# Kernel tuning notes

Hardware: AMD Instinct MI355X
Metric: run time of the kernel (lower is better)

Reference implementation:

```python
import jax, jax.numpy as jnp
import numpy as np

HEADS = 8
Q_DIM = 128
V_DIM = 128
OUT_DIM = 128
SCALE = OUT_DIM ** (-0.5)


def _lrelu(x):
    return jnp.where(x >= 0, x, 0.01 * x)


def _gelu(x):
    return jax.nn.gelu(x, approximate=False)


def setup_inputs() -> dict:
    key = jax.random.key(0)
    ks = iter(jax.random.split(key, 32))
    B, H, W, N = 4, 32, 32, 2048
    p = lambda *s: jax.random.normal(next(ks), s, dtype=jnp.float32) * 0.02
    return {
        "query": jax.random.normal(next(ks), (B, Q_DIM, H, W), dtype=jnp.float32),
        "fts": jax.random.normal(next(ks), (B * HEADS, V_DIM, N), dtype=jnp.float32),
        # 1x1 conv proj_q_c: Conv2d(q_dim, q_dim*heads)
        "wqc": p(Q_DIM * HEADS, Q_DIM), "bqc": p(Q_DIM * HEADS),
        # proj_q_l: Linear(q,q) -> LeakyReLU -> Linear(q,out) -> GELU
        "wq1": p(Q_DIM, Q_DIM), "bq1": p(Q_DIM),
        "wq2": p(OUT_DIM, Q_DIM), "bq2": p(OUT_DIM),
        # proj_k
        "wk1": p(V_DIM, V_DIM), "bk1": p(V_DIM),
        "wk2": p(OUT_DIM, V_DIM), "bk2": p(OUT_DIM),
        # proj_v
        "wv1": p(V_DIM, V_DIM), "bv1": p(V_DIM),
        "wv2": p(OUT_DIM, V_DIM), "bv2": p(OUT_DIM),
        # proj_out 1x1 conv (out_dim -> out_dim)
        "wo": p(OUT_DIM, OUT_DIM), "bo": p(OUT_DIM),
        # final_out: Linear(out*heads, out) -> LReLU -> Linear(out,out) -> LReLU
        "wf1": p(OUT_DIM, OUT_DIM * HEADS), "bf1": p(OUT_DIM),
        "wf2": p(OUT_DIM, OUT_DIM), "bf2": p(OUT_DIM),
    }


def reference(query, fts, wqc, bqc, wq1, bq1, wq2, bq2, wk1, bk1, wk2, bk2,
              wv1, bv1, wv2, bv2, wo, bo, wf1, bf1, wf2, bf2):
    B, C, H, W = query.shape
    # 1x1 conv q projection: [B, heads*q_dim, H, W]
    q1 = jnp.einsum('bchw,oc->bohw', query, wqc) + bqc[None, :, None, None]
    # rearrange 'b (h c) l w -> (b h) (l w) c'
    qh = q1.reshape(B, HEADS, C, H, W).transpose(0, 1, 3, 4, 2).reshape(B * HEADS, H * W, C)
    q = _gelu(_lrelu(qh @ wq1.T + bq1) @ wq2.T + bq2)            # [B*h, HW, D]
    ft = fts.transpose(0, 2, 1)                                   # [B*h, N, v_dim]
    k = _gelu(_lrelu(ft @ wk1.T + bk1) @ wk2.T + bk2)             # [B*h, N, D]
    v = _gelu(_lrelu(ft @ wv1.T + bv1) @ wv2.T + bv2)             # [B*h, N, D]
    attn = jax.nn.softmax(jnp.einsum('bmd,bnd->bmn', q, k) * SCALE, axis=-1)
    enh = jnp.einsum('bmn,bnd->bmd', attn, v)                     # [B*h, HW, D]
    enh4 = enh.transpose(0, 2, 1).reshape(B * HEADS, OUT_DIM, H, W)
    ho = jnp.einsum('bdhw,od->bohw', enh4, wo) + bo[None, :, None, None]
    # rearrange '(b h) c l w -> b l w (h c)'
    x = ho.reshape(B, HEADS, OUT_DIM, H, W).transpose(0, 3, 4, 1, 2).reshape(B, H, W, HEADS * OUT_DIM)
    out = _lrelu(_lrelu(x @ wf1.T + bf1) @ wf2.T + bf2)           # [B, H, W, D]
    return out
```

## Files before the change

kernel.cpp:

```cpp
#include <hip/hip_runtime.h>
#include <math.h>

typedef __attribute__((ext_vector_type(8))) __bf16 bf16x8;
typedef __attribute__((ext_vector_type(4))) float f32x4;
typedef __attribute__((ext_vector_type(4))) unsigned u32x4;

__device__ __forceinline__ float act_lrelu(float x) { return x >= 0.0f ? x : 0.01f * x; }
__device__ __forceinline__ float act_gelu(float x) { return 0.5f * x * (1.0f + erff(x * 0.7071067811865475f)); }
__device__ __forceinline__ ushort f2bf(float f) {
    unsigned u = __builtin_bit_cast(unsigned, f);
    u += 0x7fffu + ((u >> 16) & 1u);
    return (ushort)(u >> 16);
}
__device__ __forceinline__ unsigned pack2bf(float lo, float hi) {
    return (unsigned)f2bf(lo) | ((unsigned)f2bf(hi) << 16);
}

__device__ __forceinline__ void stage_wbf(const ushort* __restrict__ Wg,
                                          ushort* Wl, int tid)
{
    #pragma unroll
    for (int it = 0; it < 8; ++it) {
        const int lin = (tid + it * 256) * 8;
        const int r = lin >> 7, c = lin & 127;
        const bf16x8 v = *(const bf16x8*)&Wg[lin];
        *(bf16x8*)&Wl[r * 128 + (c ^ ((r & 7) << 3))] = v;
    }
}

__device__ __forceinline__ void layer8swz(const bf16x8 a[4], const ushort* Wl,
                                          f32x4 acc[8], int l15, int lk8)
{
    const int sx = (l15 & 7) << 3;
    #pragma unroll
    for (int ds = 0; ds < 4; ++ds) {
        const int cb = (ds * 32 + lk8) ^ sx;
        #pragma unroll
        for (int nt = 0; nt < 8; ++nt) {
            const bf16x8 b = *(const bf16x8*)&Wl[(nt * 16 + l15) * 128 + cb];
            acc[nt] = __builtin_amdgcn_mfma_f32_16x16x32_bf16(a[ds], b, acc[nt], 0, 0, 0);
        }
    }
}

template <int ACT>
__device__ __forceinline__ void retile_swz(const f32x4 acc[8], const float bias[8],
                                           ushort* tlw, int l15, int lr4, int lk8,
                                           bf16x8 aout[4])
{
    #pragma unroll
    for (int nt = 0; nt < 8; ++nt)
        #pragma unroll
        for (int j = 0; j < 4; ++j) {
            float v = acc[nt][j] + bias[nt];
            if constexpr (ACT == 1) v = act_lrelu(v);
            if constexpr (ACT == 2) v = act_gelu(v);
            const int row = lr4 + j;
            tlw[row * 128 + ((nt * 16 + l15) ^ ((row & 7) << 3))] = f2bf(v);
        }
    const int sx = (l15 & 7) << 3;
    #pragma unroll
    for (int ds = 0; ds < 4; ++ds)
        aout[ds] = *(const bf16x8*)&tlw[l15 * 128 + ((ds * 32 + lk8) ^ sx)];
}

__device__ __forceinline__ void transpose_tile(
    const float* __restrict__ IN, ushort* __restrict__ OUTb,
    int C, int N, int bx, int by, int bz, float (*T)[68], int tid)
{
    const int r = tid >> 4, c4 = (tid & 15) * 4;
    const int n0 = bx * 64, c0 = by * 64;
    const size_t ib = (size_t)bz * C * N;
    const size_t ob = (size_t)bz * N * C;
    #pragma unroll
    for (int p = 0; p < 4; ++p) {
        const int cl = r + p * 16;
        const float4 v = *(const float4*)&IN[ib + (size_t)(c0 + cl) * N + n0 + c4];
        *(float4*)&T[cl][c4] = v;
    }
    __syncthreads();
    #pragma unroll
    for (int p = 0; p < 4; ++p) {
        const int nl = r + p * 16;
        ushort4 u;
        u.x = f2bf(T[c4 + 0][nl]);
        u.y = f2bf(T[c4 + 1][nl]);
        u.z = f2bf(T[c4 + 2][nl]);
        u.w = f2bf(T[c4 + 3][nl]);
        *(ushort4*)&OUTb[ob + (size_t)(n0 + nl) * C + c0 + c4] = u;
    }
}

__global__ __launch_bounds__(256) void prep_kernel(
    const float* __restrict__ wqc, const float* __restrict__ wq1,
    const float* __restrict__ wq2, const float* __restrict__ wk1,
    const float* __restrict__ wk2, const float* __restrict__ wv1,
    const float* __restrict__ wv2, const float* __restrict__ wf2,
    const float* __restrict__ query, const float* __restrict__ fts,
    const float* __restrict__ wo, const float* __restrict__ wf1,
    const float* __restrict__ bo, const float* __restrict__ bf1,
    ushort* __restrict__ Wdst, ushort* __restrict__ queryT,
    ushort* __restrict__ ftb, ushort* __restrict__ Wcomb,
    float* __restrict__ bconst)
{
    __shared__ __align__(16) char sbuf[32768];
    const int tid = threadIdx.x;
    const int blk = blockIdx.x;

    if (blk < 60) {
        #pragma unroll
        for (int p = 0; p < 4; ++p) {
            const int lin = blk * 4096 + p * 1024 + tid * 4;
            const float* s;
            if (lin < 131072) s = wqc + lin;
            else {
                const int m = (lin - 131072) >> 14, idx = (lin - 131072) & 16383;
                s = (m == 0) ? wq1 + idx : (m == 1) ? wq2 + idx : (m == 2) ? wk1 + idx :
                    (m == 3) ? wk2 + idx : (m == 4) ? wv1 + idx : (m == 5) ? wv2 + idx
                             : wf2 + idx;
            }
            const float4 v = *(const float4*)s;
            ushort4 u; u.x = f2bf(v.x); u.y = f2bf(v.y); u.z = f2bf(v.z); u.w = f2bf(v.w);
            *(ushort4*)&Wdst[lin] = u;
        }
    } else if (blk < 188) {
        const int b2 = blk - 60;
        transpose_tile(query, queryT, 128, 1024, b2 & 15, (b2 >> 4) & 1, b2 >> 5,
                       (float(*)[68])sbuf, tid);
    } else if (blk < 196) {
        ushort* Wl = (ushort*)sbuf;
        const int h = blk - 188;
        const int lane = tid & 63, w = tid >> 6;
        const int l15 = lane & 15, lk8 = (lane >> 4) * 8, lr4 = (lane >> 4) * 4;
        #pragma unroll
        for (int it = 0; it < 16; ++it) {
            const int lin = (tid + it * 256) * 4;
            const int o = lin >> 7, d4 = lin & 127;
            const float4 v = *(const float4*)&wo[o * 128 + d4];
            #pragma unroll
            for (int j = 0; j < 4; ++j) {
                const int d = d4 + j;
                Wl[d * 128 + (o ^ ((d & 7) << 3))] = f2bf((&v.x)[j]);
            }
        }
        __syncthreads();
        const f32x4 z = {0.f, 0.f, 0.f, 0.f};
        #pragma unroll
        for (int rf = 0; rf < 2; ++rf) {
            const int row = w * 32 + rf * 16;
            bf16x8 a[4];
            #pragma unroll
            for (int ds = 0; ds < 4; ++ds) {
                const size_t base = (size_t)(row + l15) * 1024 + h * 128 + ds * 32 + lk8;
                const float4 lo = *(const float4*)&wf1[base];
                const float4 hi = *(const float4*)&wf1[base + 4];
                u32x4 wv;
                wv[0] = pack2bf(lo.x, lo.y); wv[1] = pack2bf(lo.z, lo.w);
                wv[2] = pack2bf(hi.x, hi.y); wv[3] = pack2bf(hi.z, hi.w);
                a[ds] = __builtin_bit_cast(bf16x8, wv);
            }
            f32x4 acc[8];
            #pragma unroll
            for (int i = 0; i < 8; ++i) acc[i] = z;
            layer8swz(a, Wl, acc, l15, lk8);
            #pragma unroll
            for (int nt = 0; nt < 8; ++nt)
                #pragma unroll
                for (int j = 0; j < 4; ++j)
                    Wcomb[h * 16384 + (row + lr4 + j) * 128 + nt * 16 + l15] =
                        f2bf(acc[nt][j]);
        }
    } else if (blk < 200) {
        float* sm = (float*)sbuf;
        const int jl = tid >> 3, part = tid & 7;
        const int j = (blk - 196) * 32 + jl;
        float4 a4 = {0.f, 0.f, 0.f, 0.f};
        #pragma unroll
        for (int kk = 0; kk < 128; kk += 4) {
            const float4 wv = *(const float4*)&wf1[(size_t)j * 1024 + part * 128 + kk];
            const float4 bv = *(const float4*)&bo[kk];
            a4.x += wv.x * bv.x; a4.y += wv.y * bv.y;
            a4.z += wv.z * bv.z; a4.w += wv.w * bv.w;
        }
        sm[tid] = a4.x + a4.y + a4.z + a4.w;
        __syncthreads();
        if (part == 0) {
            float t = bf1[j];
            #pragma unroll
            for (int p2 = 0; p2 < 8; ++p2) t += sm[jl * 8 + p2];
            bconst[j] = t;
        }
    } else {
        const int b2 = blk - 200;
        transpose_tile(fts, ftb, 128, 2048, b2 & 31, (b2 >> 5) & 1, b2 >> 6,
                       (float(*)[68])sbuf, tid);
    }
}

__global__ __launch_bounds__(256) void mlp1v(
    const ushort* __restrict__ X, const ushort* __restrict__ Wbf,
    const float* __restrict__ Bf, ushort* __restrict__ Y)
{
    __shared__ ushort Wl[128 * 128];
    const int tid = threadIdx.x, lane = tid & 63, w = tid >> 6;
    const int l15 = lane & 15, lk8 = (lane >> 4) * 8, lr4 = (lane >> 4) * 4;
    const int head = (blockIdx.x >> 3) & 7;
    stage_wbf(Wbf + head * 16384, Wl, tid);
    float b0[8];
    #pragma unroll
    for (int nt = 0; nt < 8; ++nt) b0[nt] = Bf[head * 128 + nt * 16 + l15];

    const int m0 = blockIdx.x * 128 + w * 32;
    bf16x8 a0[4], a1[4];
    #pragma unroll
    for (int ds = 0; ds < 4; ++ds) {
        int r0 = m0 + l15, r1 = m0 + 16 + l15;
        r0 = (r0 >> 13) * 1024 + (r0 & 1023);
        r1 = (r1 >> 13) * 1024 + (r1 & 1023);
        a0[ds] = *(const bf16x8*)(X + (size_t)r0 * 128 + ds * 32 + lk8);
        a1[ds] = *(const bf16x8*)(X + (size_t)r1 * 128 + ds * 32 + lk8);
    }
    __syncthreads();
    const f32x4 z = {0.f, 0.f, 0.f, 0.f};
    #pragma unroll
    for (int rf = 0; rf < 2; ++rf) {
        f32x4 acc[8];
        #pragma unroll
        for (int i = 0; i < 8; ++i) acc[i] = z;
        layer8swz(rf ? a1 : a0, Wl, acc, l15, lk8);
        const int row = m0 + rf * 16;
        #pragma unroll
        for (int nt = 0; nt < 8; ++nt)
            #pragma unroll
            for (int j = 0; j < 4; ++j)
                Y[(size_t)(row + lr4 + j) * 128 + nt * 16 + l15] = f2bf(acc[nt][j] + b0[nt]);
    }
}

__global__ __launch_bounds__(256) void mlp2dual(
    const ushort* __restrict__ qh, const ushort* __restrict__ ftb,
    const ushort* __restrict__ Wbf,
    const float* __restrict__ bq1, const float* __restrict__ bq2,
    const float* __restrict__ bk1, const float* __restrict__ bk2,
    const float* __restrict__ bv1, const float* __restrict__ bv2,
    ushort* __restrict__ qbuf, ushort* __restrict__ kbuf,
    ushort* __restrict__ vbufT)
{
    __shared__ ushort W1l[128 * 128], W2l[128 * 128];
    __shared__ ushort tl[4][16 * 128];
    const int tid = threadIdx.x, lane = tid & 63, w = tid >> 6;
    const int l15 = lane & 15, lk8 = (lane >> 4) * 8, lr4 = (lane >> 4) * 4;
    const int blk = blockIdx.x;

    const ushort *X, *W1, *W2;
    const float *B1, *B2;
    ushort* Y;
    bool outt = false;
    int m0;
    if (blk < 256) {
        X = qh;  W1 = Wbf + 131072; W2 = Wbf + 147456; B1 = bq1; B2 = bq2;
        Y = qbuf;  m0 = blk * 128;
    } else if (blk < 768) {
        X = ftb; W1 = Wbf + 163840; W2 = Wbf + 180224; B1 = bk1; B2 = bk2;
        Y = kbuf;  m0 = (blk - 256) * 128;
    } else {
        X = ftb; W1 = Wbf + 196608; W2 = Wbf + 212992; B1 = bv1; B2 = bv2;
        Y = vbufT; m0 = (blk - 768) * 128; outt = true;
    }
    stage_wbf(W1, W1l, tid);
    stage_wbf(W2, W2l, tid);
    float b1[8], b2[8];
    #pragma unroll
    for (int nt = 0; nt < 8; ++nt) { b1[nt] = B1[nt * 16 + l15]; b2[nt] = B2[nt * 16 + l15]; }

    const int mw = m0 + w * 32;
    bf16x8 a0[4], a1[4];
    #pragma unroll
    for (int ds = 0; ds < 4; ++ds) {
        a0[ds] = *(const bf16x8*)(X + (size_t)(mw + l15) * 128 + ds * 32 + lk8);
        a1[ds] = *(const bf16x8*)(X + (size_t)(mw + 16 + l15) * 128 + ds * 32 + lk8);
    }
    __syncthreads();
    const f32x4 z = {0.f, 0.f, 0.f, 0.f};
    #pragma unroll
    for (int rf = 0; rf < 2; ++rf) {
        const int row = mw + rf * 16;
        f32x4 acc[8];
        #pragma unroll
        for (int i = 0; i < 8; ++i) acc[i] = z;
        layer8swz(rf ? a1 : a0, W1l, acc, l15, lk8);
        bf16x8 a2[4];
        retile_swz<1>(acc, b1, tl[w], l15, lr4, lk8, a2);
        f32x4 acc2[8];
        #pragma unroll
        for (int i = 0; i < 8; ++i) acc2[i] = z;
        layer8swz(a2, W2l, acc2, l15, lk8);
        if (!outt) {
            #pragma unroll
            for (int nt = 0; nt < 8; ++nt)
                #pragma unroll
                for (int j = 0; j < 4; ++j)
                    Y[(size_t)(row + lr4 + j) * 128 + nt * 16 + l15] =
                        f2bf(act_gelu(acc2[nt][j] + b2[nt]));
        } else {
            const int R0 = row + lr4;
            const int bh = R0 >> 11, key = R0 & 2047;
            #pragma unroll
            for (int nt = 0; nt < 8; ++nt) {
                ushort4 pk;
                #pragma unroll
                for (int j = 0; j < 4; ++j)
                    (&pk.x)[j] = f2bf(act_gelu(acc2[nt][j] + b2[nt]));
                *(ushort4*)&Y[((size_t)bh * 128 + nt * 16 + l15) * 2048 + key] = pk;
            }
        }
    }
}

__global__ __launch_bounds__(128) void outpath2(
    const ushort* __restrict__ E, const ushort* __restrict__ Wcomb,
    const float* __restrict__ bconst, const ushort* __restrict__ Wf2bf,
    const float* __restrict__ Bf2, float* __restrict__ OUT)
{
    __shared__ ushort Wc[128 * 128], W2l[128 * 128];
    __shared__ ushort tl[2][16 * 128];
    const int tid = threadIdx.x, lane = tid & 63, w = tid >> 6;
    const int l15 = lane & 15, lk8 = (lane >> 4) * 8, lr4 = (lane >> 4) * 4;
    const int b = blockIdx.x >> 5;
    const int m0 = (blockIdx.x & 31) * 32;

    #pragma unroll
    for (int it = 0; it < 16; ++it) {
        const int lin = (tid + it * 128) * 8;
        const int r = lin >> 7, c = lin & 127;
        *(bf16x8*)&W2l[r * 128 + (c ^ ((r & 7) << 3))] = *(const bf16x8*)&Wf2bf[lin];
    }
    float bc[8], b2[8];
    #pragma unroll
    for (int nt = 0; nt < 8; ++nt) { bc[nt] = bconst[nt * 16 + l15]; b2[nt] = Bf2[nt * 16 + l15]; }

    const f32x4 z = {0.f, 0.f, 0.f, 0.f};
    f32x4 yacc[8];
    #pragma unroll
    for (int i = 0; i < 8; ++i) yacc[i] = z;

    bf16x8 a[4], an[4], wreg[16];
    auto loadE = [&](int h, bf16x8 dst[4]) {
        const size_t er = ((size_t)((b * 8 + h) * 1024) + m0 + w * 16 + l15) * 128;
        #pragma unroll
        for (int ds = 0; ds < 4; ++ds) dst[ds] = *(const bf16x8*)(E + er + ds * 32 + lk8);
    };
    auto wload = [&](int h) {
        #pragma unroll
        for (int it = 0; it < 16; ++it)
            wreg[it] = *(const bf16x8*)&Wcomb[h * 16384 + (tid + it * 128) * 8];
    };
    auto wwrite = [&]() {
        #pragma unroll
        for (int it = 0; it < 16; ++it) {
            const int lin = (tid + it * 128) * 8;
            const int r = lin >> 7, c = lin & 127;
            *(bf16x8*)&Wc[r * 128 + (c ^ ((r & 7) << 3))] = wreg[it];
        }
    };

    wload(0); wwrite();
    loadE(0, a);
    for (int h = 0; h < 8; ++h) {
        if (h < 7) { wload(h + 1); loadE(h + 1, an); }
        __syncthreads();
        layer8swz(a, Wc, yacc, l15, lk8);
        __syncthreads();
        if (h < 7) {
            wwrite();
            #pragma unroll
            for (int ds = 0; ds < 4; ++ds) a[ds] = an[ds];
        }
    }
    bf16x8 a3[4];
    retile_swz<1>(yacc, bc, tl[w], l15, lr4, lk8, a3);
    f32x4 oacc[8];
    #pragma unroll
    for (int i = 0; i < 8; ++i) oacc[i] = z;
    layer8swz(a3, W2l, oacc, l15, lk8);
    #pragma unroll
    for (int nt = 0; nt < 8; ++nt)
        #pragma unroll
        for (int j = 0; j < 4; ++j)
            OUT[((size_t)b * 1024 + m0 + w * 16 + lr4 + j) * 128 + nt * 16 + l15] =
                act_lrelu(oacc[nt][j] + b2[nt]);
}

__global__ __launch_bounds__(256, 3) void flash_attn_bf16(
    const ushort* __restrict__ Q, const ushort* __restrict__ Kx,
    const ushort* __restrict__ Vt, ushort* __restrict__ O)
{
    constexpr float SCALE = 0.08838834764831845f;
    const int bid = blockIdx.x;
    const int bh = (bid & 7) * 4 + ((bid >> 3) & 3);
    const int m0 = (bid >> 5) * 64;
    const int tid = threadIdx.x;
    const int lane = tid & 63, w = tid >> 6;
    const int l15 = lane & 15, g = lane >> 4;
    const int lk8 = g * 8, lr4 = g * 4;
    const int sxk = (l15 & 7) << 3;
    const int sel = g >> 1;
    const int src0 = l15 + ((lane & 16) << 1);

    __shared__ ushort K_lds[2][64 * 128];
    __shared__ ushort V_lds[128 * 64];

    const ushort* Qb = Q + (size_t)bh * 1024 * 128;
    const ushort* Kb = Kx + (size_t)bh * 2048 * 128;
    const ushort* Vb = Vt + (size_t)bh * 128 * 2048;

    bf16x8 qf[4];
    {
        const int row = m0 + w * 16 + l15;
        #pragma unroll
        for (int ds = 0; ds < 4; ++ds)
            qf[ds] = *(const bf16x8*)(Qb + (size_t)row * 128 + ds * 32 + lk8);
    }

    const int kr = tid >> 4, kc = (tid & 15) * 8;
    const int vr = tid >> 3, vc = (tid & 7) * 8;
    bf16x8 kreg[4], vreg[4];
    #pragma unroll
    for (int it = 0; it < 4; ++it) {
        kreg[it] = *(const bf16x8*)(Kb + (size_t)(kr + it * 16) * 128 + kc);
        vreg[it] = *(const bf16x8*)(Vb + (size_t)(vr + it * 32) * 2048 + vc);
    }
    #pragma unroll
    for (int it = 0; it < 4; ++it) {
        const int r = kr + it * 16;
        *(bf16x8*)&K_lds[0][r * 128 + (kc ^ ((r & 7) << 3))] = kreg[it];
        const int rv = vr + it * 32;
        *(bf16x8*)&V_lds[rv * 64 + (vc ^ ((rv & 7) << 3))] = vreg[it];
    }
    __syncthreads();

    f32x4 oacc[8];
    #pragma unroll
    for (int i = 0; i < 8; ++i) oacc[i] = f32x4{0.f, 0.f, 0.f, 0.f};
    float mrun = -1e30f, lrun = 0.f;
    int cur = 0;

    for (int nt = 0; nt < 32; ++nt) {
        if (nt < 31) {
            const int n1 = (nt + 1) * 64;
            #pragma unroll
            for (int it = 0; it < 4; ++it) {
                kreg[it] = *(const bf16x8*)(Kb + (size_t)(n1 + kr + it * 16) * 128 + kc);
                vreg[it] = *(const bf16x8*)(Vb + (size_t)(vr + it * 32) * 2048 + n1 + vc);
            }
        }
        const ushort* Kc = &K_lds[cur][0];

        f32x4 s[4];
        #pragma unroll
        for (int i = 0; i < 4; ++i) s[i] = f32x4{0.f, 0.f, 0.f, 0.f};
        __builtin_amdgcn_s_setprio(1);
        #pragma unroll
        for (int ds = 0; ds < 4; ++ds)
            #pragma unroll
            for (int ct = 0; ct < 4; ++ct) {
                const bf16x8 kf = *(const bf16x8*)
                    &Kc[(ct * 16 + l15) * 128 + ((ds * 32 + lk8) ^ sxk)];
                s[ct] = __builtin_amdgcn_mfma_f32_16x16x32_bf16(kf, qf[ds], s[ct], 0, 0, 0);
            }
        __builtin_amdgcn_s_setprio(0);

        float mx = fmaxf(fmaxf(fmaxf(s[0][0], s[0][1]), fmaxf(s[0][2], s[0][3])),
                         fmaxf(fmaxf(s[1][0], s[1][1]), fmaxf(s[1][2], s[1][3])));
        mx = fmaxf(mx, fmaxf(fmaxf(fmaxf(s[2][0], s[2][1]), fmaxf(s[2][2], s[2][3])),
                             fmaxf(fmaxf(s[3][0], s[3][1]), fmaxf(s[3][2], s[3][3]))));
        mx *= SCALE;
        mx = fmaxf(mx, __shfl_xor(mx, 16));
        mx = fmaxf(mx, __shfl_xor(mx, 32));

        if (!__all((int)(mx <= mrun + 8.f))) {
            const float mnew = fmaxf(mrun, mx);
            const float fsc = __expf(mrun - mnew);
            mrun = mnew;
            lrun *= fsc;
            #pragma unroll
            for (int dt = 0; dt < 8; ++dt)
                #pragma unroll
                for (int j = 0; j < 4; ++j)
                    oacc[dt][j] *= fsc;
        }

        float p[4][4];
        float sum = 0.f;
        #pragma unroll
        for (int ct = 0; ct < 4; ++ct)
            #pragma unroll
            for (int r = 0; r < 4; ++r) {
                const float e = __expf(s[ct][r] * SCALE - mrun);
                p[ct][r] = e;
                sum += e;
            }
        sum += __shfl_xor(sum, 16);
        sum += __shfl_xor(sum, 32);
        lrun += sum;

        unsigned P2[4][2];
        #pragma unroll
        for (int ct = 0; ct < 4; ++ct) {
            P2[ct][0] = pack2bf(p[ct][0], p[ct][1]);
            P2[ct][1] = pack2bf(p[ct][2], p[ct][3]);
        }

        __builtin_amdgcn_s_setprio(1);
        #pragma unroll
        for (int ks = 0; ks < 2; ++ks) {
            u32x4 wv;
            #pragma unroll
            for (int t = 0; t < 4; ++t) {
                const int src = src0 + ((t >> 1) << 4);
                const unsigned wa = __shfl(P2[ks * 2 + 0][t & 1], src);
                const unsigned wb = __shfl(P2[ks * 2 + 1][t & 1], src);
                wv[t] = sel ? wb : wa;
            }
            const bf16x8 pa = __builtin_bit_cast(bf16x8, wv);
            #pragma unroll
            for (int dt = 0; dt < 8; ++dt) {
                const int rv = dt * 16 + l15;
                const bf16x8 vb = *(const bf16x8*)
                    &V_lds[rv * 64 + ((ks * 32 + lk8) ^ sxk)];
                oacc[dt] = __builtin_amdgcn_mfma_f32_16x16x32_bf16(vb, pa, oacc[dt], 0, 0, 0);
            }
        }
        __builtin_amdgcn_s_setprio(0);

        if (nt < 31) {
            __syncthreads();
            const int nxt = cur ^ 1;
            #pragma unroll
            for (int it = 0; it < 4; ++it) {
                const int r = kr + it * 16;
                *(bf16x8*)&K_lds[nxt][r * 128 + (kc ^ ((r & 7) << 3))] = kreg[it];
                const int rv = vr + it * 32;
                *(bf16x8*)&V_lds[rv * 64 + (vc ^ ((rv & 7) << 3))] = vreg[it];
            }
            __syncthreads();
            cur ^= 1;
        }
    }

    ushort* Ob = O + ((size_t)bh * 1024 + m0 + w * 16 + l15) * 128;
    const float inv = 1.0f / lrun;
    #pragma unroll
    for (int dt = 0; dt < 8; ++dt) {
        ushort4 pk;
        #pragma unroll
        for (int r = 0; r < 4; ++r) (&pk.x)[r] = f2bf(oacc[dt][r] * inv);
        *(ushort4*)&Ob[dt * 16 + lr4] = pk;
    }
}

extern "C" void kernel_launch(void* const* d_in, const int* in_sizes, int n_in,
                              void* d_out, int out_size, void* d_ws, size_t ws_size,
                              hipStream_t stream)
{
    (void)in_sizes; (void)n_in; (void)out_size; (void)ws_size;
    const float* query = (const float*)d_in[0];
    const float* fts   = (const float*)d_in[1];
    const float* wqc = (const float*)d_in[2];
    const float* bqc = (const float*)d_in[3];
    const float* wq1 = (const float*)d_in[4];
    const float* bq1 = (const float*)d_in[5];
    const float* wq2 = (const float*)d_in[6];
    const float* bq2 = (const float*)d_in[7];
    const float* wk1 = (const float*)d_in[8];
    const float* bk1 = (const float*)d_in[9];
    const float* wk2 = (const float*)d_in[10];
    const float* bk2 = (const float*)d_in[11];
    const float* wv1 = (const float*)d_in[12];
    const float* bv1 = (const float*)d_in[13];
    const float* wv2 = (const float*)d_in[14];
    const float* bv2 = (const float*)d_in[15];
    const float* wo  = (const float*)d_in[16];
    const float* bo  = (const float*)d_in[17];
    const float* wf1 = (const float*)d_in[18];
    const float* bf1 = (const float*)d_in[19];
    const float* wf2 = (const float*)d_in[20];
    const float* bf2 = (const float*)d_in[21];
    float* out = (float*)d_out;

    char* ws = (char*)d_ws;
    ushort* ftb    = (ushort*)(ws + 0LL);
    ushort* queryT = (ushort*)(ws + 16777216LL);
    ushort* qh     = (ushort*)(ws + 17825792LL);
    ushort* qbuf   = (ushort*)(ws + 26214400LL);
    ushort* kbuf   = (ushort*)(ws + 34603008LL);
    ushort* vbufT  = (ushort*)(ws + 51380224LL);
    ushort* enh    = (ushort*)(ws + 68157440LL);
    ushort* Wbf    = (ushort*)(ws + 76546048LL);
    ushort* Wcomb  = (ushort*)(ws + 77299712LL);
    float*  bconst = (float*) (ws + 77561856LL);

    ushort* wqc_b = Wbf + 0;
    ushort* wf2_b = Wbf + 229376;

    prep_kernel<<<2248, 256, 0, stream>>>(
        wqc, wq1, wq2, wk1, wk2, wv1, wv2, wf2, query, fts, wo, wf1, bo, bf1,
        Wbf, queryT, ftb, Wcomb, bconst);
    mlp1v<<<256, 256, 0, stream>>>(queryT, wqc_b, bqc, qh);
    mlp2dual<<<1280, 256, 0, stream>>>(qh, ftb, Wbf, bq1, bq2, bk1, bk2,
                                       bv1, bv2, qbuf, kbuf, vbufT);
    flash_attn_bf16<<<512, 256, 0, stream>>>(qbuf, kbuf, vbufT, enh);
    outpath2<<<128, 128, 0, stream>>>(enh, Wcomb, bconst, wf2_b, bf2, out);
}
```

Measured before the change: 182.6 us.

## Fuse q conv projection into the q MLP and split k/v MLPs into separate launches

The 1x1 conv q projection is fused with both q MLP layers into one kernel, so the qh intermediate no longer goes to global memory. The k and v MLPs become a templated kernel launched twice. Blocks grow to 512 threads covering 256 rows, and the second row-fragment's input is prefetched while the first is computed. This removes one kernel's round trip through global memory and some weight restaging, but uses more LDS per block (up to about 128KB for the q kernel), which may lower occupancy, and adds an extra launch for the k/v split.

```diff
diff --git a/kernel.cpp b/kernel.cpp
--- a/kernel.cpp
+++ b/kernel.cpp
@@ -22,6 +22,18 @@
     #pragma unroll
     for (int it = 0; it < 8; ++it) {
         const int lin = (tid + it * 256) * 8;
+        const int r = lin >> 7, c = lin & 127;
+        const bf16x8 v = *(const bf16x8*)&Wg[lin];
+        *(bf16x8*)&Wl[r * 128 + (c ^ ((r & 7) << 3))] = v;
+    }
+}
+
+__device__ __forceinline__ void stage_wbf512(const ushort* __restrict__ Wg,
+                                             ushort* Wl, int tid)
+{
+    #pragma unroll
+    for (int it = 0; it < 4; ++it) {
+        const int lin = (tid + it * 512) * 8;
         const int r = lin >> 7, c = lin & 127;
         const bf16x8 v = *(const bf16x8*)&Wg[lin];
         *(bf16x8*)&Wl[r * 128 + (c ^ ((r & 7) << 3))] = v;
@@ -197,105 +209,114 @@
     }
 }
 
-__global__ __launch_bounds__(256) void mlp1v(
-    const ushort* __restrict__ X, const ushort* __restrict__ Wbf,
-    const float* __restrict__ Bf, ushort* __restrict__ Y)
-{
-    __shared__ ushort Wl[128 * 128];
+__global__ __launch_bounds__(512) void mlp3q(
+    const ushort* __restrict__ Xq, const ushort* __restrict__ Wbf,
+    const float* __restrict__ Bqc, const float* __restrict__ B1,
+    const float* __restrict__ B2, ushort* __restrict__ Y)
+{
+    __shared__ ushort W0l[128 * 128], W1l[128 * 128], W2l[128 * 128];
+    __shared__ ushort tl[8][16 * 128];
     const int tid = threadIdx.x, lane = tid & 63, w = tid >> 6;
     const int l15 = lane & 15, lk8 = (lane >> 4) * 8, lr4 = (lane >> 4) * 4;
-    const int head = (blockIdx.x >> 3) & 7;
-    stage_wbf(Wbf + head * 16384, Wl, tid);
-    float b0[8];
-    #pragma unroll
-    for (int nt = 0; nt < 8; ++nt) b0[nt] = Bf[head * 128 + nt * 16 + l15];
-
-    const int m0 = blockIdx.x * 128 + w * 32;
-    bf16x8 a0[4], a1[4];
-    #pragma unroll
-    for (int ds = 0; ds < 4; ++ds) {
-        int r0 = m0 + l15, r1 = m0 + 16 + l15;
-        r0 = (r0 >> 13) * 1024 + (r0 & 1023);
-        r1 = (r1 >> 13) * 1024 + (r1 & 1023);
-        a0[ds] = *(const bf16x8*)(X + (size_t)r0 * 128 + ds * 32 + lk8);
-        a1[ds] = *(const bf16x8*)(X + (size_t)r1 * 128 + ds * 32 + lk8);
+    const int head = (blockIdx.x >> 2) & 7;
+    stage_wbf512(Wbf + head * 16384, W0l, tid);
+    stage_wbf512(Wbf + 131072, W1l, tid);
+    stage_wbf512(Wbf + 147456, W2l, tid);
+    float b0[8], b1[8], b2[8];
+    #pragma unroll
+    for (int nt = 0; nt < 8; ++nt) {
+        b0[nt] = Bqc[head * 128 + nt * 16 + l15];
+        b1[nt] = B1[nt * 16 + l15];
+        b2[nt] = B2[nt * 16 + l15];
+    }
+
+    const int m0 = blockIdx.x * 256 + w * 32;
+    bf16x8 a[4], an[4];
+    {
+        const int r = (m0 >> 13) * 1024 + (m0 & 1023) + l15;
+        #pragma unroll
+        for (int ds = 0; ds < 4; ++ds)
+            a[ds] = *(const bf16x8*)(Xq + (size_t)r * 128 + ds * 32 + lk8);
     }
     __syncthreads();
     const f32x4 z = {0.f, 0.f, 0.f, 0.f};
     #pragma unroll
     for (int rf = 0; rf < 2; ++rf) {
+        const int row = m0 + rf * 16;
+        if (rf < 1) {
+            const int r = ((row + 16) >> 13) * 1024 + ((row + 16) & 1023) + l15;
+            #pragma unroll
+            for (int ds = 0; ds < 4; ++ds)
+                an[ds] = *(const bf16x8*)(Xq + (size_t)r * 128 + ds * 32 + lk8);
+        }
         f32x4 acc[8];
         #pragma unroll
         for (int i = 0; i < 8; ++i) acc[i] = z;
-        layer8swz(rf ? a1 : a0, Wl, acc, l15, lk8);
-        const int row = m0 + rf * 16;
+        layer8swz(a, W0l, acc, l15, lk8);
+        bf16x8 a1[4];
+        retile_swz<0>(acc, b0, tl[w], l15, lr4, lk8, a1);
+        #pragma unroll
+        for (int i = 0; i < 8; ++i) acc[i] = z;
+        layer8swz(a1, W1l, acc, l15, lk8);
+        bf16x8 a2[4];
+        retile_swz<1>(acc, b1, tl[w], l15, lr4, lk8, a2);
+        #pragma unroll
+        for (int i = 0; i < 8; ++i) acc[i] = z;
+        layer8swz(a2, W2l, acc, l15, lk8);
         #pragma unroll
         for (int nt = 0; nt < 8; ++nt)
             #pragma unroll
             for (int j = 0; j < 4; ++j)
-                Y[(size_t)(row + lr4 + j) * 128 + nt * 16 + l15] = f2bf(acc[nt][j] + b0[nt]);
-    }
-}
-
-__global__ __launch_bounds__(256) void mlp2dual(
-    const ushort* __restrict__ qh, const ushort* __restrict__ ftb,
-    const ushort* __restrict__ Wbf,
-    const float* __restrict__ bq1, const float* __restrict__ bq2,
-    const float* __restrict__ bk1, const float* __restrict__ bk2,
-    const float* __restrict__ bv1, const float* __restrict__ bv2,
-    ushort* __restrict__ qbuf, ushort* __restrict__ kbuf,
-    ushort* __restrict__ vbufT)
+                Y[(size_t)(row + lr4 + j) * 128 + nt * 16 + l15] =
+                    f2bf(act_gelu(acc[nt][j] + b2[nt]));
+        #pragma unroll
+        for (int ds = 0; ds < 4; ++ds) a[ds] = an[ds];
+    }
+}
+
+template <bool OUTT>
+__global__ __launch_bounds__(512) void mlp2v(
+    const ushort* __restrict__ X,
+    const ushort* __restrict__ W1bf, const float* __restrict__ B1,
+    const ushort* __restrict__ W2bf, const float* __restrict__ B2,
+    ushort* __restrict__ Y)
 {
     __shared__ ushort W1l[128 * 128], W2l[128 * 128];
-    __shared__ ushort tl[4][16 * 128];
+    __shared__ ushort tl[8][16 * 128];
     const int tid = threadIdx.x, lane = tid & 63, w = tid >> 6;
     const int l15 = lane & 15, lk8 = (lane >> 4) * 8, lr4 = (lane >> 4) * 4;
-    const int blk = blockIdx.x;
-
-    const ushort *X, *W1, *W2;
-    const float *B1, *B2;
-    ushort* Y;
-    bool outt = false;
-    int m0;
-    if (blk < 256) {
-        X = qh;  W1 = Wbf + 131072; W2 = Wbf + 147456; B1 = bq1; B2 = bq2;
-        Y = qbuf;  m0 = blk * 128;
-    } else if (blk < 768) {
-        X = ftb; W1 = Wbf + 163840; W2 = Wbf + 180224; B1 = bk1; B2 = bk2;
-        Y = kbuf;  m0 = (blk - 256) * 128;
-    } else {
-        X = ftb; W1 = Wbf + 196608; W2 = Wbf + 212992; B1 = bv1; B2 = bv2;
-        Y = vbufT; m0 = (blk - 768) * 128; outt = true;
-    }
-    stage_wbf(W1, W1l, tid);
-    stage_wbf(W2, W2l, tid);
+    stage_wbf512(W1bf, W1l, tid);
+    stage_wbf512(W2bf, W2l, tid);
     float b1[8], b2[8];
     #pragma unroll
     for (int nt = 0; nt < 8; ++nt) { b1[nt] = B1[nt * 16 + l15]; b2[nt] = B2[nt * 16 + l15]; }
 
-    const int mw = m0 + w * 32;
-    bf16x8 a0[4], a1[4];
-    #pragma unroll
-    for (int ds = 0; ds < 4; ++ds) {
-        a0[ds] = *(const bf16x8*)(X + (size_t)(mw + l15) * 128 + ds * 32 + lk8);
-        a1[ds] = *(const bf16x8*)(X + (size_t)(mw + 16 + l15) * 128 + ds * 32 + lk8);
-    }
+    const int m0 = blockIdx.x * 256 + w * 32;
+    bf16x8 a[4], an[4];
+    #pragma unroll
+    for (int ds = 0; ds < 4; ++ds)
+        a[ds] = *(const bf16x8*)(X + (size_t)(m0 + l15) * 128 + ds * 32 + lk8);
     __syncthreads();
     const f32x4 z = {0.f, 0.f, 0.f, 0.f};
     #pragma unroll
     for (int rf = 0; rf < 2; ++rf) {
-        const int row = mw + rf * 16;
+        const int row = m0 + rf * 16;
+        if (rf < 1) {
+            #pragma unroll
+            for (int ds = 0; ds < 4; ++ds)
+                an[ds] = *(const bf16x8*)(X + (size_t)(row + 16 + l15) * 128 + ds * 32 + lk8);
+        }
         f32x4 acc[8];
         #pragma unroll
         for (int i = 0; i < 8; ++i) acc[i] = z;
-        layer8swz(rf ? a1 : a0, W1l, acc, l15, lk8);
+        layer8swz(a, W1l, acc, l15, lk8);
         bf16x8 a2[4];
         retile_swz<1>(acc, b1, tl[w], l15, lr4, lk8, a2);
         f32x4 acc2[8];
         #pragma unroll
         for (int i = 0; i < 8; ++i) acc2[i] = z;
         layer8swz(a2, W2l, acc2, l15, lk8);
-        if (!outt) {
+        if constexpr (!OUTT) {
             #pragma unroll
             for (int nt = 0; nt < 8; ++nt)
                 #pragma unroll
@@ -314,6 +335,8 @@
                 *(ushort4*)&Y[((size_t)bh * 128 + nt * 16 + l15) * 2048 + key] = pk;
             }
         }
+        #pragma unroll
+        for (int ds = 0; ds < 4; ++ds) a[ds] = an[ds];
     }
 }
 
@@ -591,7 +614,6 @@
     char* ws = (char*)d_ws;
     ushort* ftb    = (ushort*)(ws + 0LL);
     ushort* queryT = (ushort*)(ws + 16777216LL);
-    ushort* qh     = (ushort*)(ws + 17825792LL);
     ushort* qbuf   = (ushort*)(ws + 26214400LL);
     ushort* kbuf   = (ushort*)(ws + 34603008LL);
     ushort* vbufT  = (ushort*)(ws + 51380224LL);
@@ -600,15 +622,14 @@
     ushort* Wcomb  = (ushort*)(ws + 77299712LL);
     float*  bconst = (float*) (ws + 77561856LL);
 
-    ushort* wqc_b = Wbf + 0;
     ushort* wf2_b = Wbf + 229376;
 
     prep_kernel<<<2248, 256, 0, stream>>>(
         wqc, wq1, wq2, wk1, wk2, wv1, wv2, wf2, query, fts, wo, wf1, bo, bf1,
         Wbf, queryT, ftb, Wcomb, bconst);
-    mlp1v<<<256, 256, 0, stream>>>(queryT, wqc_b, bqc, qh);
-    mlp2dual<<<1280, 256, 0, stream>>>(qh, ftb, Wbf, bq1, bq2, bk1, bk2,
-                                       bv1, bv2, qbuf, kbuf, vbufT);
+    mlp3q<<<128, 512, 0, stream>>>(queryT, Wbf, bqc, bq1, bq2, qbuf);
+    mlp2v<false><<<256, 512, 0, stream>>>(ftb, Wbf + 163840, bk1, Wbf + 180224, bk2, kbuf);
+    mlp2v<true><<<256, 512, 0, stream>>>(ftb, Wbf + 196608, bv1, Wbf + 212992, bv2, vbufT);
     flash_attn_bf16<<<512, 256, 0, stream>>>(qbuf, kbuf, vbufT, enh);
     outpath2<<<128, 128, 0, stream>>>(enh, Wcomb, bconst, wf2_b, bf2, out);
 }
```

New measurement: 311.0 us. 1.7x slower.

## Split attention over key halves with combine kernel; split fused MLP launch into three

Applied to the files above, without the earlier changes.

The flash attention kernel now splits the 2048 keys into two halves, launching 1024 blocks instead of 512. Each block writes unnormalized fp32 partial outputs plus running max/sum, and a new combine kernel merges them with log-sum-exp weights into the bf16 output. The aim is more parallelism and better CU fill on the attention stage. The cost is roughly 32 MB of extra fp32 partial traffic and one more launch. The merged q/k/v MLP kernel is also replaced by three launches of a templated kernel, which removes the per-block branch but serializes the launches.

```diff
diff --git a/kernel.cpp b/kernel.cpp
--- a/kernel.cpp
+++ b/kernel.cpp
@@ -237,54 +237,35 @@
     }
 }
 
-__global__ __launch_bounds__(256) void mlp2dual(
-    const ushort* __restrict__ qh, const ushort* __restrict__ ftb,
-    const ushort* __restrict__ Wbf,
-    const float* __restrict__ bq1, const float* __restrict__ bq2,
-    const float* __restrict__ bk1, const float* __restrict__ bk2,
-    const float* __restrict__ bv1, const float* __restrict__ bv2,
-    ushort* __restrict__ qbuf, ushort* __restrict__ kbuf,
-    ushort* __restrict__ vbufT)
+template <bool OUTT>
+__global__ __launch_bounds__(256) void mlp2v(
+    const ushort* __restrict__ X,
+    const ushort* __restrict__ W1bf, const float* __restrict__ B1,
+    const ushort* __restrict__ W2bf, const float* __restrict__ B2,
+    ushort* __restrict__ Y)
 {
     __shared__ ushort W1l[128 * 128], W2l[128 * 128];
     __shared__ ushort tl[4][16 * 128];
     const int tid = threadIdx.x, lane = tid & 63, w = tid >> 6;
     const int l15 = lane & 15, lk8 = (lane >> 4) * 8, lr4 = (lane >> 4) * 4;
-    const int blk = blockIdx.x;
-
-    const ushort *X, *W1, *W2;
-    const float *B1, *B2;
-    ushort* Y;
-    bool outt = false;
-    int m0;
-    if (blk < 256) {
-        X = qh;  W1 = Wbf + 131072; W2 = Wbf + 147456; B1 = bq1; B2 = bq2;
-        Y = qbuf;  m0 = blk * 128;
-    } else if (blk < 768) {
-        X = ftb; W1 = Wbf + 163840; W2 = Wbf + 180224; B1 = bk1; B2 = bk2;
-        Y = kbuf;  m0 = (blk - 256) * 128;
-    } else {
-        X = ftb; W1 = Wbf + 196608; W2 = Wbf + 212992; B1 = bv1; B2 = bv2;
-        Y = vbufT; m0 = (blk - 768) * 128; outt = true;
-    }
-    stage_wbf(W1, W1l, tid);
-    stage_wbf(W2, W2l, tid);
+    stage_wbf(W1bf, W1l, tid);
+    stage_wbf(W2bf, W2l, tid);
     float b1[8], b2[8];
     #pragma unroll
     for (int nt = 0; nt < 8; ++nt) { b1[nt] = B1[nt * 16 + l15]; b2[nt] = B2[nt * 16 + l15]; }
 
-    const int mw = m0 + w * 32;
+    const int m0 = blockIdx.x * 128 + w * 32;
     bf16x8 a0[4], a1[4];
     #pragma unroll
     for (int ds = 0; ds < 4; ++ds) {
-        a0[ds] = *(const bf16x8*)(X + (size_t)(mw + l15) * 128 + ds * 32 + lk8);
-        a1[ds] = *(const bf16x8*)(X + (size_t)(mw + 16 + l15) * 128 + ds * 32 + lk8);
+        a0[ds] = *(const bf16x8*)(X + (size_t)(m0 + l15) * 128 + ds * 32 + lk8);
+        a1[ds] = *(const bf16x8*)(X + (size_t)(m0 + 16 + l15) * 128 + ds * 32 + lk8);
     }
     __syncthreads();
     const f32x4 z = {0.f, 0.f, 0.f, 0.f};
     #pragma unroll
     for (int rf = 0; rf < 2; ++rf) {
-        const int row = mw + rf * 16;
+        const int row = m0 + rf * 16;
         f32x4 acc[8];
         #pragma unroll
         for (int i = 0; i < 8; ++i) acc[i] = z;
@@ -295,7 +276,7 @@
         #pragma unroll
         for (int i = 0; i < 8; ++i) acc2[i] = z;
         layer8swz(a2, W2l, acc2, l15, lk8);
-        if (!outt) {
+        if constexpr (!OUTT) {
             #pragma unroll
             for (int nt = 0; nt < 8; ++nt)
                 #pragma unroll
@@ -391,14 +372,17 @@
                 act_lrelu(oacc[nt][j] + b2[nt]);
 }
 
-__global__ __launch_bounds__(256, 3) void flash_attn_bf16(
+__global__ __launch_bounds__(256, 3) void flash_part(
     const ushort* __restrict__ Q, const ushort* __restrict__ Kx,
-    const ushort* __restrict__ Vt, ushort* __restrict__ O)
+    const ushort* __restrict__ Vt, float* __restrict__ Op,
+    float2* __restrict__ ml)
 {
     constexpr float SCALE = 0.08838834764831845f;
     const int bid = blockIdx.x;
     const int bh = (bid & 7) * 4 + ((bid >> 3) & 3);
-    const int m0 = (bid >> 5) * 64;
+    const int ks_half = (bid >> 5) & 1;
+    const int m0 = (bid >> 6) * 64;
+    const int n00 = ks_half * 1024;
     const int tid = threadIdx.x;
     const int lane = tid & 63, w = tid >> 6;
     const int l15 = lane & 15, g = lane >> 4;
@@ -427,8 +411,8 @@
     bf16x8 kreg[4], vreg[4];
     #pragma unroll
     for (int it = 0; it < 4; ++it) {
-        kreg[it] = *(const bf16x8*)(Kb + (size_t)(kr + it * 16) * 128 + kc);
-        vreg[it] = *(const bf16x8*)(Vb + (size_t)(vr + it * 32) * 2048 + vc);
+        kreg[it] = *(const bf16x8*)(Kb + (size_t)(n00 + kr + it * 16) * 128 + kc);
+        vreg[it] = *(const bf16x8*)(Vb + (size_t)(vr + it * 32) * 2048 + n00 + vc);
     }
     #pragma unroll
     for (int it = 0; it < 4; ++it) {
@@ -445,9 +429,9 @@
     float mrun = -1e30f, lrun = 0.f;
     int cur = 0;
 
-    for (int nt = 0; nt < 32; ++nt) {
-        if (nt < 31) {
-            const int n1 = (nt + 1) * 64;
+    for (int nt = 0; nt < 16; ++nt) {
+        if (nt < 15) {
+            const int n1 = n00 + (nt + 1) * 64;
             #pragma unroll
             for (int it = 0; it < 4; ++it) {
                 kreg[it] = *(const bf16x8*)(Kb + (size_t)(n1 + kr + it * 16) * 128 + kc);
@@ -533,7 +517,7 @@
         }
         __builtin_amdgcn_s_setprio(0);
 
-        if (nt < 31) {
+        if (nt < 15) {
             __syncthreads();
             const int nxt = cur ^ 1;
             #pragma unroll
@@ -548,15 +532,43 @@
         }
     }
 
-    ushort* Ob = O + ((size_t)bh * 1024 + m0 + w * 16 + l15) * 128;
-    const float inv = 1.0f / lrun;
-    #pragma unroll
-    for (int dt = 0; dt < 8; ++dt) {
-        ushort4 pk;
-        #pragma unroll
-        for (int r = 0; r < 4; ++r) (&pk.x)[r] = f2bf(oacc[dt][r] * inv);
-        *(ushort4*)&Ob[dt * 16 + lr4] = pk;
-    }
+    const int row = m0 + w * 16 + l15;
+    float* Ob = Op + (size_t)ks_half * 4194304 + ((size_t)bh * 1024 + row) * 128;
+    #pragma unroll
+    for (int dt = 0; dt < 8; ++dt)
+        *(f32x4*)&Ob[dt * 16 + lr4] = oacc[dt];
+    if (g == 0)
+        ml[(size_t)ks_half * 32768 + bh * 1024 + row] = float2{mrun, lrun};
+}
+
+__global__ __launch_bounds__(256) void combine_kernel(
+    const float* __restrict__ Op, const float2* __restrict__ ml,
+    ushort* __restrict__ enh)
+{
+    const int t = threadIdx.x;
+    const int row = blockIdx.x * 16 + (t >> 4);
+    const int d = (t & 15) * 8;
+    const float2 a = ml[row];
+    const float2 b = ml[32768 + row];
+    const float m = fmaxf(a.x, b.x);
+    const float w1 = __expf(a.x - m), w2 = __expf(b.x - m);
+    const float inv = 1.0f / (a.y * w1 + b.y * w2);
+    const size_t off = (size_t)row * 128 + d;
+    const float4 o1a = *(const float4*)&Op[off];
+    const float4 o1b = *(const float4*)&Op[off + 4];
+    const float4 o2a = *(const float4*)&Op[4194304 + off];
+    const float4 o2b = *(const float4*)&Op[4194304 + off + 4];
+    ushort4 u0, u1;
+    u0.x = f2bf((o1a.x * w1 + o2a.x * w2) * inv);
+    u0.y = f2bf((o1a.y * w1 + o2a.y * w2) * inv);
+    u0.z = f2bf((o1a.z * w1 + o2a.z * w2) * inv);
+    u0.w = f2bf((o1a.w * w1 + o2a.w * w2) * inv);
+    u1.x = f2bf((o1b.x * w1 + o2b.x * w2) * inv);
+    u1.y = f2bf((o1b.y * w1 + o2b.y * w2) * inv);
+    u1.z = f2bf((o1b.z * w1 + o2b.z * w2) * inv);
+    u1.w = f2bf((o1b.w * w1 + o2b.w * w2) * inv);
+    *(ushort4*)&enh[off] = u0;
+    *(ushort4*)&enh[off + 4] = u1;
 }
 
 extern "C" void kernel_launch(void* const* d_in, const int* in_sizes, int n_in,
@@ -599,6 +611,8 @@
     ushort* Wbf    = (ushort*)(ws + 76546048LL);
     ushort* Wcomb  = (ushort*)(ws + 77299712LL);
     float*  bconst = (float*) (ws + 77561856LL);
+    float*  Opart  = (float*) (ws + 83886080LL);
+    float2* mlbuf  = (float2*)(ws + 117440512LL);
 
     ushort* wqc_b = Wbf + 0;
     ushort* wf2_b = Wbf + 229376;
@@ -607,8 +621,10 @@
         wqc, wq1, wq2, wk1, wk2, wv1, wv2, wf2, query, fts, wo, wf1, bo, bf1,
         Wbf, queryT, ftb, Wcomb, bconst);
     mlp1v<<<256, 256, 0, stream>>>(queryT, wqc_b, bqc, qh);
-    mlp2dual<<<1280, 256, 0, stream>>>(qh, ftb, Wbf, bq1, bq2, bk1, bk2,
-                                       bv1, bv2, qbuf, kbuf, vbufT);
-    flash_attn_bf16<<<512, 256, 0, stream>>>(qbuf, kbuf, vbufT, enh);
+    mlp2v<false><<<256, 256, 0, stream>>>(qh, Wbf + 131072, bq1, Wbf + 147456, bq2, qbuf);
+    mlp2v<false><<<512, 256, 0, stream>>>(ftb, Wbf + 163840, bk1, Wbf + 180224, bk2, kbuf);
+    mlp2v<true><<<512, 256, 0, stream>>>(ftb, Wbf + 196608, bv1, Wbf + 212992, bv2, vbufT);
+    flash_part<<<1024, 256, 0, stream>>>(qbuf, kbuf, vbufT, Opart, mlbuf);
+    combine_kernel<<<2048, 256, 0, stream>>>(Opart, mlbuf, enh);
     outpath2<<<128, 128, 0, stream>>>(enh, Wcomb, bconst, wf2_b, bf2, out);
 }
```

Measured after the change: 225.9 us. 23.7% more time.

## Split fused two-layer MLP kernel into two single-layer launches

Applied to the files above, without the earlier changes.

Replaces the fused two-layer q/k/v MLP kernel with a templated single-layer kernel launched twice. The intermediate activations go through a new global scratch buffer instead of an in-register/LDS retile. Each block now stages one 32KB weight tile instead of two, which lowers LDS use and may raise occupancy. In exchange it adds extra global traffic for the intermediate (about 40MB written and read back) and one more kernel launch.

```diff
diff --git a/kernel.cpp b/kernel.cpp
--- a/kernel.cpp
+++ b/kernel.cpp
@@ -237,41 +237,38 @@
     }
 }
 
-__global__ __launch_bounds__(256) void mlp2dual(
-    const ushort* __restrict__ qh, const ushort* __restrict__ ftb,
-    const ushort* __restrict__ Wbf,
-    const float* __restrict__ bq1, const float* __restrict__ bq2,
-    const float* __restrict__ bk1, const float* __restrict__ bk2,
-    const float* __restrict__ bv1, const float* __restrict__ bv2,
-    ushort* __restrict__ qbuf, ushort* __restrict__ kbuf,
-    ushort* __restrict__ vbufT)
-{
-    __shared__ ushort W1l[128 * 128], W2l[128 * 128];
-    __shared__ ushort tl[4][16 * 128];
+template <int ACT, bool VOUTT>
+__global__ __launch_bounds__(256) void mlpL(
+    const ushort* __restrict__ Xq, const ushort* __restrict__ Xk,
+    const ushort* __restrict__ Xv, const ushort* __restrict__ Wbf,
+    int woq, int wok, int wov,
+    const float* __restrict__ Bq, const float* __restrict__ Bk,
+    const float* __restrict__ Bv,
+    ushort* __restrict__ Yq, ushort* __restrict__ Yk, ushort* __restrict__ Yv)
+{
+    __shared__ ushort Wl[128 * 128];
     const int tid = threadIdx.x, lane = tid & 63, w = tid >> 6;
     const int l15 = lane & 15, lk8 = (lane >> 4) * 8, lr4 = (lane >> 4) * 4;
     const int blk = blockIdx.x;
 
-    const ushort *X, *W1, *W2;
-    const float *B1, *B2;
+    const ushort* X;
+    const float* B;
     ushort* Y;
     bool outt = false;
     int m0;
     if (blk < 256) {
-        X = qh;  W1 = Wbf + 131072; W2 = Wbf + 147456; B1 = bq1; B2 = bq2;
-        Y = qbuf;  m0 = blk * 128;
+        X = Xq; B = Bq; Y = Yq; m0 = blk * 128;
+        stage_wbf(Wbf + woq, Wl, tid);
     } else if (blk < 768) {
-        X = ftb; W1 = Wbf + 163840; W2 = Wbf + 180224; B1 = bk1; B2 = bk2;
-        Y = kbuf;  m0 = (blk - 256) * 128;
+        X = Xk; B = Bk; Y = Yk; m0 = (blk - 256) * 128;
+        stage_wbf(Wbf + wok, Wl, tid);
     } else {
-        X = ftb; W1 = Wbf + 196608; W2 = Wbf + 212992; B1 = bv1; B2 = bv2;
-        Y = vbufT; m0 = (blk - 768) * 128; outt = true;
-    }
-    stage_wbf(W1, W1l, tid);
-    stage_wbf(W2, W2l, tid);
-    float b1[8], b2[8];
-    #pragma unroll
-    for (int nt = 0; nt < 8; ++nt) { b1[nt] = B1[nt * 16 + l15]; b2[nt] = B2[nt * 16 + l15]; }
+        X = Xv; B = Bv; Y = Yv; m0 = (blk - 768) * 128; outt = VOUTT;
+        stage_wbf(Wbf + wov, Wl, tid);
+    }
+    float b[8];
+    #pragma unroll
+    for (int nt = 0; nt < 8; ++nt) b[nt] = B[nt * 16 + l15];
 
     const int mw = m0 + w * 32;
     bf16x8 a0[4], a1[4];
@@ -288,20 +285,16 @@
         f32x4 acc[8];
         #pragma unroll
         for (int i = 0; i < 8; ++i) acc[i] = z;
-        layer8swz(rf ? a1 : a0, W1l, acc, l15, lk8);
-        bf16x8 a2[4];
-        retile_swz<1>(acc, b1, tl[w], l15, lr4, lk8, a2);
-        f32x4 acc2[8];
-        #pragma unroll
-        for (int i = 0; i < 8; ++i) acc2[i] = z;
-        layer8swz(a2, W2l, acc2, l15, lk8);
+        layer8swz(rf ? a1 : a0, Wl, acc, l15, lk8);
         if (!outt) {
             #pragma unroll
             for (int nt = 0; nt < 8; ++nt)
                 #pragma unroll
-                for (int j = 0; j < 4; ++j)
-                    Y[(size_t)(row + lr4 + j) * 128 + nt * 16 + l15] =
-                        f2bf(act_gelu(acc2[nt][j] + b2[nt]));
+                for (int j = 0; j < 4; ++j) {
+                    float v = acc[nt][j] + b[nt];
+                    v = (ACT == 1) ? act_lrelu(v) : act_gelu(v);
+                    Y[(size_t)(row + lr4 + j) * 128 + nt * 16 + l15] = f2bf(v);
+                }
         } else {
             const int R0 = row + lr4;
             const int bh = R0 >> 11, key = R0 & 2047;
@@ -309,8 +302,11 @@
             for (int nt = 0; nt < 8; ++nt) {
                 ushort4 pk;
                 #pragma unroll
-                for (int j = 0; j < 4; ++j)
-                    (&pk.x)[j] = f2bf(act_gelu(acc2[nt][j] + b2[nt]));
+                for (int j = 0; j < 4; ++j) {
+                    float v = acc[nt][j] + b[nt];
+                    v = (ACT == 1) ? act_lrelu(v) : act_gelu(v);
+                    (&pk.x)[j] = f2bf(v);
+                }
                 *(ushort4*)&Y[((size_t)bh * 128 + nt * 16 + l15) * 2048 + key] = pk;
             }
         }
@@ -599,16 +595,22 @@
     ushort* Wbf    = (ushort*)(ws + 76546048LL);
     ushort* Wcomb  = (ushort*)(ws + 77299712LL);
     float*  bconst = (float*) (ws + 77561856LL);
+    ushort* tbuf   = (ushort*)(ws + 83886080LL);
 
     ushort* wqc_b = Wbf + 0;
     ushort* wf2_b = Wbf + 229376;
+    ushort* tq = tbuf;
+    ushort* tk = tbuf + (size_t)32768 * 128;
+    ushort* tv = tbuf + (size_t)98304 * 128;
 
     prep_kernel<<<2248, 256, 0, stream>>>(
         wqc, wq1, wq2, wk1, wk2, wv1, wv2, wf2, query, fts, wo, wf1, bo, bf1,
         Wbf, queryT, ftb, Wcomb, bconst);
     mlp1v<<<256, 256, 0, stream>>>(queryT, wqc_b, bqc, qh);
-    mlp2dual<<<1280, 256, 0, stream>>>(qh, ftb, Wbf, bq1, bq2, bk1, bk2,
-                                       bv1, bv2, qbuf, kbuf, vbufT);
+    mlpL<1, false><<<1280, 256, 0, stream>>>(
+        qh, ftb, ftb, Wbf, 131072, 163840, 196608, bq1, bk1, bv1, tq, tk, tv);
+    mlpL<2, true><<<1280, 256, 0, stream>>>(
+        tq, tk, tv, Wbf, 147456, 180224, 212992, bq2, bk2, bv2, qbuf, kbuf, vbufT);
     flash_attn_bf16<<<512, 256, 0, stream>>>(qbuf, kbuf, vbufT, enh);
     outpath2<<<128, 128, 0, stream>>>(enh, Wcomb, bconst, wf2_b, bf2, out);
 }
```

Result: slower. 189.8 us (+4.0%).
